# Kernel optimization log

Measured on AMD Instinct MI355X. Metric: run time of the kernel, lower is better.

## Reference

```python
import jax, jax.numpy as jnp
import numpy as np

NUM_HEADS = 16
ROPE_THETA = 10000.0


def apply_rope(x):
    # x: (B, H, T, hd), interleaved-pair RoPE (rotary-embedding-torch convention)
    T, hd = x.shape[-2], x.shape[-1]
    inv_freq = 1.0 / (ROPE_THETA ** (jnp.arange(0, hd, 2, dtype=jnp.float32) / hd))  # (hd/2,)
    ang = jnp.arange(T, dtype=jnp.float32)[:, None] * inv_freq[None, :]  # (T, hd/2)
    cos, sin = jnp.cos(ang), jnp.sin(ang)
    x1 = x[..., 0::2]
    x2 = x[..., 1::2]
    r1 = x1 * cos - x2 * sin
    r2 = x1 * sin + x2 * cos
    return jnp.stack([r1, r2], axis=-1).reshape(x.shape)


def setup_inputs() -> dict:
    key = jax.random.key(0)
    ks = jax.random.split(key, 8)
    L, S, B, E = 2048, 2048, 2, 1024
    sc = 1.0 / np.sqrt(E)
    return {
        "query": jax.random.normal(ks[0], (L, B, E), jnp.float32),
        "key": jax.random.normal(ks[1], (S, B, E), jnp.float32),
        "value": jax.random.normal(ks[2], (S, B, E), jnp.float32),
        "key_padding_mask": jnp.zeros((B, S), dtype=bool),
        "Wq": jax.random.normal(ks[3], (E, E), jnp.float32) * sc,
        "bq": jnp.zeros((E,), jnp.float32),
        "Wk": jax.random.normal(ks[4], (E, E), jnp.float32) * sc,
        "bk": jnp.zeros((E,), jnp.float32),
        "Wv": jax.random.normal(ks[5], (E, E), jnp.float32) * sc,
        "bv": jnp.zeros((E,), jnp.float32),
        "Wo": jax.random.normal(ks[6], (E, E), jnp.float32) * sc,
        "bo": jnp.zeros((E,), jnp.float32),
    }


def reference(query, key, value, key_padding_mask, Wq, bq, Wk, bk, Wv, bv, Wo, bo):
    L, B, E = query.shape
    S = key.shape[0]
    H = NUM_HEADS
    hd = E // H
    # projections (torch Linear: x @ W.T + b)
    Q = query @ Wq.T + bq  # (L, B, E)
    K = key @ Wk.T + bk    # (S, B, E)
    V = value @ Wv.T + bv  # (S, B, E)
    # (T, B, E) -> (B, H, T, hd)
    Q = Q.reshape(L, B, H, hd).transpose(1, 2, 0, 3)
    K = K.reshape(S, B, H, hd).transpose(1, 2, 0, 3)
    V = V.reshape(S, B, H, hd).transpose(1, 2, 0, 3)
    Q = apply_rope(Q)
    K = apply_rope(K)
    scores = jnp.einsum("bhld,bhsd->bhls", Q, K) / jnp.sqrt(jnp.float32(hd))
    scores = jnp.where(key_padding_mask[:, None, None, :], -jnp.inf, scores)
    attn = jax.nn.softmax(scores, axis=-1)
    out = jnp.einsum("bhls,bhsd->bhld", attn, V)  # (B, H, L, hd)
    out = out.transpose(2, 0, 1, 3).reshape(L, B, E)
    return out @ Wo.T + bo
```

## Files before the change

kernel.cpp:

```cpp
#include <hip/hip_runtime.h>
#include <hip/hip_bf16.h>

typedef __hip_bfloat16 bf16;
typedef short bf16x8 __attribute__((ext_vector_type(8)));
typedef float f32x4 __attribute__((ext_vector_type(4)));
typedef short s4 __attribute__((ext_vector_type(4)));

#define LL 2048
#define SS 2048
#define EE 1024
#define HH 16
#define HD 64
#define MM (LL * 2)

static __device__ __forceinline__ short f2bs(float f) {
  bf16 h = __float2bfloat16(f);
  short u;
  __builtin_memcpy(&u, &h, 2);
  return u;
}

#define GLL16(gp, lp) __builtin_amdgcn_global_load_lds(                        \
    (const __attribute__((address_space(1))) void*)(gp),                       \
    (__attribute__((address_space(3))) void*)(lp), 16, 0, 0)

__global__ __launch_bounds__(256) void rope_table_kernel(float2* __restrict__ tab) {
  int i = blockIdx.x * 256 + threadIdx.x;
  int pos = i >> 5, fi = i & 31;
  float freq = expf(-(float)fi * (9.210340371976184f / 32.0f));
  float ang = (float)pos * freq;
  float s, c;
  sincosf(ang, &s, &c);
  tab[i] = make_float2(c, s);
}

__global__ void maskf_kernel(const unsigned char* __restrict__ m,
                             float* __restrict__ mf) {
  int i = blockIdx.x * 256 + threadIdx.x;
  if (i < 2 * SS) mf[i] = m[i] ? -1e30f : 0.f;
}

__global__ __launch_bounds__(256) void cvt_kernel(const float* __restrict__ src,
                                                  bf16* __restrict__ dst) {
  size_t i = ((size_t)blockIdx.x * 256 + threadIdx.x) * 4;
  float4 v = *(const float4*)(src + i);
  s4 p;
  p[0] = f2bs(v.x); p[1] = f2bs(v.y); p[2] = f2bs(v.z); p[3] = f2bs(v.w);
  *(s4*)(dst + i) = p;
}

template<int MODE, bool XB16, bool WB16>
__global__ __launch_bounds__(256) void proj_kernel(
    const void* __restrict__ Xv, const void* __restrict__ Wv,
    const float* __restrict__ bias, void* __restrict__ dstv,
    const float2* __restrict__ tab)
{
  const int w = threadIdx.x >> 6;
  const int lane = threadIdx.x & 63;
  const int l15 = lane & 15, quad = lane >> 4;
  const int tm = blockIdx.x * 128 + w * 32;
  const int tn = blockIdx.y * 64;

  const size_t aoff0 = (size_t)(tm + l15) * EE + quad * 8;
  const size_t aoff1 = aoff0 + (size_t)16 * EE;
  const size_t woff  = (size_t)(tn + l15) * EE + quad * 8;

  f32x4 zero4 = {0.f, 0.f, 0.f, 0.f};
  f32x4 acc[2][4];
#pragma unroll
  for (int mi = 0; mi < 2; ++mi)
#pragma unroll
    for (int ni = 0; ni < 4; ++ni) acc[mi][ni] = zero4;

  for (int k0 = 0; k0 < EE; k0 += 32) {
    bf16x8 a0, a1;
    if (XB16 || MODE == 3) {
      const bf16* Xb = (const bf16*)Xv;
      a0 = *(const bf16x8*)(Xb + aoff0 + k0);
      a1 = *(const bf16x8*)(Xb + aoff1 + k0);
    } else {
      const float* Xf = (const float*)Xv;
#pragma unroll
      for (int j = 0; j < 8; ++j) a0[j] = f2bs(Xf[aoff0 + k0 + j]);
#pragma unroll
      for (int j = 0; j < 8; ++j) a1[j] = f2bs(Xf[aoff1 + k0 + j]);
    }
#pragma unroll
    for (int ni = 0; ni < 4; ++ni) {
      bf16x8 bv;
      if (WB16) {
        const bf16* Wb = (const bf16*)Wv;
        bv = *(const bf16x8*)(Wb + woff + (size_t)ni * 16 * EE + k0);
      } else {
        const float* Wf = (const float*)Wv;
#pragma unroll
        for (int j = 0; j < 8; ++j) bv[j] = f2bs(Wf[woff + (size_t)ni * 16 * EE + k0 + j]);
      }
      acc[0][ni] = __builtin_amdgcn_mfma_f32_16x16x32_bf16(a0, bv, acc[0][ni], 0, 0, 0);
      acc[1][ni] = __builtin_amdgcn_mfma_f32_16x16x32_bf16(a1, bv, acc[1][ni], 0, 0, 0);
    }
  }

  float bz[4];
#pragma unroll
  for (int ni = 0; ni < 4; ++ni) bz[ni] = bias[tn + ni * 16 + l15];

#pragma unroll
  for (int mi = 0; mi < 2; ++mi) {
#pragma unroll
    for (int ni = 0; ni < 4; ++ni) {
      const int n = tn + ni * 16 + l15;
#pragma unroll
      for (int r = 0; r < 4; ++r) {
        const int m = tm + mi * 16 + quad * 4 + r;
        float v = acc[mi][ni][r] + bz[ni];
        if (MODE <= 1) {
          float other = __shfl_xor(v, 1, 64);
          int pos = m >> 1, b = m & 1, d = n & 63, h = n >> 6;
          float2 cs = tab[pos * 32 + (d >> 1)];
          float rv = (d & 1) ? (other * cs.y + v * cs.x) : (v * cs.x - other * cs.y);
          ((bf16*)dstv)[((size_t)(b * HH + h) * LL + pos) * HD + d] = __float2bfloat16(rv);
        } else if (MODE == 2) {
          int pos = m >> 1, b = m & 1, d = n & 63, h = n >> 6;
          ((bf16*)dstv)[((size_t)(b * HH + h) * HD + d) * SS + pos] = __float2bfloat16(v);
        } else {
          ((float*)dstv)[(size_t)m * EE + n] = v;
        }
      }
    }
  }
}

template<int MODE>
__global__ __launch_bounds__(256) void projs_kernel(
    const bf16* __restrict__ X, const bf16* __restrict__ W,
    const float* __restrict__ bias, void* __restrict__ dstv,
    const float2* __restrict__ tab)
{
  __shared__ __align__(16) bf16 As[128 * 32];
  __shared__ __align__(16) bf16 Bs[64 * 32];

  const int tid = threadIdx.x;
  const int w = tid >> 6;
  const int lane = tid & 63;
  const int l15 = lane & 15, quad = lane >> 4;
  const int tmb = blockIdx.x * 128;
  const int tm  = tmb + w * 32;
  const int tn  = blockIdx.y * 64;

  const int srow = tid >> 2;
  const int schk = tid & 3;
  const int gc8  = (schk ^ ((srow >> 1) & 3)) * 8;
  const int swz  = (quad ^ ((l15 >> 1) & 3)) * 8;

  const bf16* gA0 = X + (size_t)(tmb + srow) * EE + gc8;
  const bf16* gA1 = X + (size_t)(tmb + 64 + srow) * EE + gc8;
  const bf16* gB  = W + (size_t)(tn + srow) * EE + gc8;
  bf16* lA0 = As + srow * 32 + schk * 8;
  bf16* lA1 = As + (64 + srow) * 32 + schk * 8;
  bf16* lB  = Bs + srow * 32 + schk * 8;

  f32x4 zero4 = {0.f, 0.f, 0.f, 0.f};
  f32x4 acc[2][4];
#pragma unroll
  for (int mi = 0; mi < 2; ++mi)
#pragma unroll
    for (int ni = 0; ni < 4; ++ni) acc[mi][ni] = zero4;

  for (int k0 = 0; k0 < EE; k0 += 32) {
    GLL16(gA0 + k0, lA0);
    GLL16(gA1 + k0, lA1);
    GLL16(gB + k0, lB);
    __syncthreads();
    bf16x8 af0 = *(const bf16x8*)(As + (w * 32 + l15) * 32 + swz);
    bf16x8 af1 = *(const bf16x8*)(As + (w * 32 + 16 + l15) * 32 + swz);
#pragma unroll
    for (int ni = 0; ni < 4; ++ni) {
      bf16x8 bfr = *(const bf16x8*)(Bs + (ni * 16 + l15) * 32 + swz);
      acc[0][ni] = __builtin_amdgcn_mfma_f32_16x16x32_bf16(af0, bfr, acc[0][ni], 0, 0, 0);
      acc[1][ni] = __builtin_amdgcn_mfma_f32_16x16x32_bf16(af1, bfr, acc[1][ni], 0, 0, 0);
    }
    __syncthreads();
  }

  float bz[4];
#pragma unroll
  for (int ni = 0; ni < 4; ++ni) bz[ni] = bias[tn + ni * 16 + l15];

#pragma unroll
  for (int mi = 0; mi < 2; ++mi) {
#pragma unroll
    for (int ni = 0; ni < 4; ++ni) {
      const int n = tn + ni * 16 + l15;
#pragma unroll
      for (int r = 0; r < 4; ++r) {
        const int m = tm + mi * 16 + quad * 4 + r;
        float v = acc[mi][ni][r] + bz[ni];
        if (MODE <= 1) {
          float other = __shfl_xor(v, 1, 64);
          int pos = m >> 1, b = m & 1, d = n & 63, h = n >> 6;
          float2 cs = tab[pos * 32 + (d >> 1)];
          float rv = (d & 1) ? (other * cs.y + v * cs.x) : (v * cs.x - other * cs.y);
          ((bf16*)dstv)[((size_t)(b * HH + h) * LL + pos) * HD + d] = __float2bfloat16(rv);
        } else if (MODE == 2) {
          int pos = m >> 1, b = m & 1, d = n & 63, h = n >> 6;
          ((bf16*)dstv)[((size_t)(b * HH + h) * HD + d) * SS + pos] = __float2bfloat16(v);
        } else {
          ((float*)dstv)[(size_t)m * EE + n] = v;
        }
      }
    }
  }
}

__global__ __launch_bounds__(256) void attn_kernel(
    const bf16* __restrict__ Qr, const bf16* __restrict__ Kr,
    const bf16* __restrict__ Vt, const float* __restrict__ maskf,
    bf16* __restrict__ ctx)
{
  __shared__ __align__(16) bf16 Ks[2][64 * 64];
  __shared__ __align__(16) bf16 Vs[2][64 * 64];
  __shared__ __align__(16) short Plds[4][32][56];

  const int w = threadIdx.x >> 6;
  const int lane = threadIdx.x & 63;
  const int l15 = lane & 15, quad = lane >> 4;
  const int id = blockIdx.x;
  const int bh = id & 31;
  const int qt = id >> 5;
  const int b = bh >> 4, h = bh & 15;
  const int q0 = qt * 128 + w * 32;

  const bf16* Qbh = Qr + (size_t)bh * LL * HD;
  const bf16* Kbh = Kr + (size_t)bh * SS * HD;
  const bf16* Vbh = Vt + (size_t)bh * HD * SS;
  const float* mrow = maskf + b * SS;

  bf16x8 qf[2][2];
#pragma unroll
  for (int mi = 0; mi < 2; ++mi) {
    const bf16* qp = Qbh + (size_t)(q0 + mi * 16 + l15) * HD + quad * 8;
    qf[mi][0] = *(const bf16x8*)(qp);
    qf[mi][1] = *(const bf16x8*)(qp + 32);
  }

  const int srow = lane >> 3;
  const int gswz = ((lane & 7) ^ srow) * 8;
  const int kswz0 = ((quad    ) ^ (l15 & 7)) * 8;
  const int kswz1 = ((quad + 4) ^ (l15 & 7)) * 8;

#define STAGE(buf, S0) {                                                       \
    _Pragma("unroll")                                                          \
    for (int i = 0; i < 2; ++i) {                                              \
      const int rb = w * 16 + i * 8;                                           \
      GLL16(Kbh + (size_t)((S0) + rb + srow) * HD + gswz,                      \
            (bf16*)&Ks[buf][rb * 64] + lane * 8);                              \
      GLL16(Vbh + (size_t)(rb + srow) * SS + (S0) + gswz,                      \
            (bf16*)&Vs[buf][rb * 64] + lane * 8);                              \
    }                                                                          \
  }

  f32x4 zero4 = {0.f, 0.f, 0.f, 0.f};
  f32x4 o[2][4];
#pragma unroll
  for (int mi = 0; mi < 2; ++mi)
#pragma unroll
    for (int t = 0; t < 4; ++t) o[mi][t] = zero4;
  float ps0 = 0.f, ps1 = 0.f;

  STAGE(0, 0);
  __syncthreads();

  for (int t = 0; t < SS / 64; ++t) {
    const int s0 = t * 64;
    const int cur = t & 1;
    if (t + 1 < SS / 64) STAGE(cur ^ 1, s0 + 64);

#pragma unroll
    for (int ss = 0; ss < 2; ++ss) {
      const bf16* Kb = &Ks[cur][ss * 32 * 64];
      bf16x8 kf00 = *(const bf16x8*)(Kb + (l15)      * 64 + kswz0);
      bf16x8 kf01 = *(const bf16x8*)(Kb + (l15)      * 64 + kswz1);
      bf16x8 kf10 = *(const bf16x8*)(Kb + (16 + l15) * 64 + kswz0);
      bf16x8 kf11 = *(const bf16x8*)(Kb + (16 + l15) * 64 + kswz1);
      bf16x8 vf[4];
#pragma unroll
      for (int tt = 0; tt < 4; ++tt)
        vf[tt] = *(const bf16x8*)(&Vs[cur][0] + (tt * 16 + l15) * 64 +
                                  (((ss * 4 + quad) ^ (l15 & 7)) * 8));
      f32x4 mv0 = *(const f32x4*)(mrow + s0 + ss * 32 + quad * 4);
      f32x4 mv1 = *(const f32x4*)(mrow + s0 + ss * 32 + 16 + quad * 4);

#pragma unroll
      for (int mi = 0; mi < 2; ++mi) {
        f32x4 sc0 = zero4, sc1 = zero4;
        sc0 = __builtin_amdgcn_mfma_f32_16x16x32_bf16(kf00, qf[mi][0], sc0, 0, 0, 0);
        sc0 = __builtin_amdgcn_mfma_f32_16x16x32_bf16(kf01, qf[mi][1], sc0, 0, 0, 0);
        sc1 = __builtin_amdgcn_mfma_f32_16x16x32_bf16(kf10, qf[mi][0], sc1, 0, 0, 0);
        sc1 = __builtin_amdgcn_mfma_f32_16x16x32_bf16(kf11, qf[mi][1], sc1, 0, 0, 0);
        s4 pk0, pk1;
#pragma unroll
        for (int r = 0; r < 4; ++r) {
          float p = __expf(sc0[r] * 0.125f + mv0[r]);
          if (mi == 0) ps0 += p; else ps1 += p;
          pk0[r] = f2bs(p);
        }
#pragma unroll
        for (int r = 0; r < 4; ++r) {
          float p = __expf(sc1[r] * 0.125f + mv1[r]);
          if (mi == 0) ps0 += p; else ps1 += p;
          pk1[r] = f2bs(p);
        }
        *(s4*)&Plds[w][mi * 16 + l15][quad * 4] = pk0;
        *(s4*)&Plds[w][mi * 16 + l15][16 + quad * 4] = pk1;
      }
      asm volatile("" ::: "memory");
      bf16x8 pf0 = *(const bf16x8*)&Plds[w][l15][quad * 8];
      bf16x8 pf1 = *(const bf16x8*)&Plds[w][16 + l15][quad * 8];
#pragma unroll
      for (int tt = 0; tt < 4; ++tt) {
        o[0][tt] = __builtin_amdgcn_mfma_f32_16x16x32_bf16(pf0, vf[tt], o[0][tt], 0, 0, 0);
        o[1][tt] = __builtin_amdgcn_mfma_f32_16x16x32_bf16(pf1, vf[tt], o[1][tt], 0, 0, 0);
      }
      asm volatile("" ::: "memory");
    }
    __syncthreads();
  }
#undef STAGE

  float lv0 = ps0; lv0 += __shfl_xor(lv0, 16, 64); lv0 += __shfl_xor(lv0, 32, 64);
  float lv1 = ps1; lv1 += __shfl_xor(lv1, 16, 64); lv1 += __shfl_xor(lv1, 32, 64);

#pragma unroll
  for (int mi = 0; mi < 2; ++mi) {
#pragma unroll
    for (int r = 0; r < 4; ++r) {
      float lv = (mi == 0) ? lv0 : lv1;
      float li = __shfl(lv, quad * 4 + r, 64);
      float inv = 1.0f / li;
      int q = q0 + mi * 16 + quad * 4 + r;
#pragma unroll
      for (int t = 0; t < 4; ++t) {
        float val = o[mi][t][r] * inv;
        ctx[(size_t)(q * 2 + b) * EE + (size_t)h * 64 + t * 16 + l15] = __float2bfloat16(val);
      }
    }
  }
}

extern "C" void kernel_launch(void* const* d_in, const int* in_sizes, int n_in,
                              void* d_out, int out_size, void* d_ws, size_t ws_size,
                              hipStream_t stream) {
  const float* query = (const float*)d_in[0];
  const float* key   = (const float*)d_in[1];
  const float* value = (const float*)d_in[2];
  const unsigned char* mask = (const unsigned char*)d_in[3];
  const float* Wq = (const float*)d_in[4];
  const float* bq = (const float*)d_in[5];
  const float* Wk = (const float*)d_in[6];
  const float* bk = (const float*)d_in[7];
  const float* Wv = (const float*)d_in[8];
  const float* bv = (const float*)d_in[9];
  const float* Wo = (const float*)d_in[10];
  const float* bo = (const float*)d_in[11];

  char* ws = (char*)d_ws;
  const bool big = ws_size >= ((size_t)41 << 20);

  float2* tab   = (float2*)ws;
  float*  maskf = (float*)(ws + (512 << 10));
  bf16* Wb = (bf16*)(ws + ((size_t)1 << 20));
  bf16* Xb = (bf16*)(ws + ((size_t)9 << 20));
  size_t base = big ? ((size_t)17 << 20) : ((size_t)1 << 20);
  bf16* Qr  = (bf16*)(ws + base);
  bf16* Kr  = (bf16*)(ws + base + ((size_t)8 << 20));
  bf16* Vt  = (bf16*)(ws + base + ((size_t)16 << 20));
  bf16* ctx = big ? Xb : (bf16*)(ws + ((size_t)25 << 20));

  rope_table_kernel<<<(LL * 32) / 256, 256, 0, stream>>>(tab);
  maskf_kernel<<<16, 256, 0, stream>>>(mask, maskf);

  dim3 gp(MM / 128, EE / 64);
  if (big) {
    cvt_kernel<<<1024, 256, 0, stream>>>(Wq, Wb);
    cvt_kernel<<<1024, 256, 0, stream>>>(Wk, Wb + (size_t)EE * EE);
    cvt_kernel<<<1024, 256, 0, stream>>>(Wv, Wb + (size_t)2 * EE * EE);
    cvt_kernel<<<1024, 256, 0, stream>>>(Wo, Wb + (size_t)3 * EE * EE);
    cvt_kernel<<<4096, 256, 0, stream>>>(query, Xb);
    projs_kernel<0><<<gp, 256, 0, stream>>>(Xb, Wb, bq, Qr, tab);
    cvt_kernel<<<4096, 256, 0, stream>>>(key, Xb);
    projs_kernel<1><<<gp, 256, 0, stream>>>(Xb, Wb + (size_t)EE * EE, bk, Kr, tab);
    cvt_kernel<<<4096, 256, 0, stream>>>(value, Xb);
    projs_kernel<2><<<gp, 256, 0, stream>>>(Xb, Wb + (size_t)2 * EE * EE, bv, Vt, tab);
  } else {
    proj_kernel<0, false, false><<<gp, 256, 0, stream>>>(query, Wq, bq, Qr, tab);
    proj_kernel<1, false, false><<<gp, 256, 0, stream>>>(key,   Wk, bk, Kr, tab);
    proj_kernel<2, false, false><<<gp, 256, 0, stream>>>(value, Wv, bv, Vt, tab);
  }

  attn_kernel<<<(LL / 128) * 2 * HH, 256, 0, stream>>>(Qr, Kr, Vt, maskf, ctx);

  if (big) projs_kernel<3><<<gp, 256, 0, stream>>>(ctx, Wb + (size_t)3 * EE * EE, bo, d_out, tab);
  else     proj_kernel<3, true, false><<<gp, 256, 0, stream>>>(ctx, Wo, bo, d_out, tab);
}
```

Baseline: 270.7 us.

## Double-buffer projection GEMM with 64-wide K tiles and fuse setup kernels

The shared-memory projection GEMM now uses two LDS buffers with a K tile of 64 instead of 32, prefetching the next tile via global_load_lds while the current one feeds MFMAs. This halves the number of K-loop iterations, cuts the barriers per iteration from two to one, and hides global load latency. It uses a new XOR swizzle across 8 chunks and more LDS. Separately, the rope-table and mask kernels are merged into one launch, and the four weight conversions are merged into a single cvt4 launch to reduce launch overhead.

Result: no change. 265.9 us (-1.8%).

```diff
diff --git a/kernel.cpp b/kernel.cpp
--- a/kernel.cpp
+++ b/kernel.cpp
@@ -24,20 +24,21 @@
     (const __attribute__((address_space(1))) void*)(gp),                       \
     (__attribute__((address_space(3))) void*)(lp), 16, 0, 0)
 
-__global__ __launch_bounds__(256) void rope_table_kernel(float2* __restrict__ tab) {
-  int i = blockIdx.x * 256 + threadIdx.x;
-  int pos = i >> 5, fi = i & 31;
-  float freq = expf(-(float)fi * (9.210340371976184f / 32.0f));
-  float ang = (float)pos * freq;
-  float s, c;
-  sincosf(ang, &s, &c);
-  tab[i] = make_float2(c, s);
-}
-
-__global__ void maskf_kernel(const unsigned char* __restrict__ m,
-                             float* __restrict__ mf) {
-  int i = blockIdx.x * 256 + threadIdx.x;
-  if (i < 2 * SS) mf[i] = m[i] ? -1e30f : 0.f;
+__global__ __launch_bounds__(256) void tables_kernel(
+    float2* __restrict__ tab, const unsigned char* __restrict__ m,
+    float* __restrict__ mf) {
+  if (blockIdx.x < 256) {
+    int i = blockIdx.x * 256 + threadIdx.x;
+    int pos = i >> 5, fi = i & 31;
+    float freq = expf(-(float)fi * (9.210340371976184f / 32.0f));
+    float ang = (float)pos * freq;
+    float s, c;
+    sincosf(ang, &s, &c);
+    tab[i] = make_float2(c, s);
+  } else {
+    int i = (blockIdx.x - 256) * 256 + threadIdx.x;
+    if (i < 2 * SS) mf[i] = m[i] ? -1e30f : 0.f;
+  }
 }
 
 __global__ __launch_bounds__(256) void cvt_kernel(const float* __restrict__ src,
@@ -47,6 +48,19 @@
   s4 p;
   p[0] = f2bs(v.x); p[1] = f2bs(v.y); p[2] = f2bs(v.z); p[3] = f2bs(v.w);
   *(s4*)(dst + i) = p;
+}
+
+__global__ __launch_bounds__(256) void cvt4_kernel(
+    const float* __restrict__ s0, const float* __restrict__ s1,
+    const float* __restrict__ s2, const float* __restrict__ s3,
+    bf16* __restrict__ dst) {
+  int sel = blockIdx.x >> 10;
+  const float* src = (sel == 0) ? s0 : (sel == 1) ? s1 : (sel == 2) ? s2 : s3;
+  size_t loc = ((size_t)(blockIdx.x & 1023) * 256 + threadIdx.x) * 4;
+  float4 v = *(const float4*)(src + loc);
+  s4 p;
+  p[0] = f2bs(v.x); p[1] = f2bs(v.y); p[2] = f2bs(v.z); p[3] = f2bs(v.w);
+  *(s4*)(dst + (size_t)sel * EE * EE + loc) = p;
 }
 
 template<int MODE, bool XB16, bool WB16>
@@ -137,8 +151,8 @@
     const float* __restrict__ bias, void* __restrict__ dstv,
     const float2* __restrict__ tab)
 {
-  __shared__ __align__(16) bf16 As[128 * 32];
-  __shared__ __align__(16) bf16 Bs[64 * 32];
+  __shared__ __align__(16) bf16 As[2][128 * 64];
+  __shared__ __align__(16) bf16 Bs[2][64 * 64];
 
   const int tid = threadIdx.x;
   const int w = tid >> 6;
@@ -148,17 +162,23 @@
   const int tm  = tmb + w * 32;
   const int tn  = blockIdx.y * 64;
 
-  const int srow = tid >> 2;
-  const int schk = tid & 3;
-  const int gc8  = (schk ^ ((srow >> 1) & 3)) * 8;
-  const int swz  = (quad ^ ((l15 >> 1) & 3)) * 8;
-
-  const bf16* gA0 = X + (size_t)(tmb + srow) * EE + gc8;
-  const bf16* gA1 = X + (size_t)(tmb + 64 + srow) * EE + gc8;
-  const bf16* gB  = W + (size_t)(tn + srow) * EE + gc8;
-  bf16* lA0 = As + srow * 32 + schk * 8;
-  bf16* lA1 = As + (64 + srow) * 32 + schk * 8;
-  bf16* lB  = Bs + srow * 32 + schk * 8;
+  const int srow = lane >> 3;
+  const int sgc  = ((lane & 7) ^ srow) * 8;
+
+#define PSTAGE(buf, K0) {                                                      \
+    _Pragma("unroll")                                                          \
+    for (int i = 0; i < 4; ++i) {                                              \
+      const int rb = w * 32 + i * 8;                                           \
+      GLL16(X + (size_t)(tmb + rb + srow) * EE + (K0) + sgc,                   \
+            (bf16*)&As[buf][rb * 64] + lane * 8);                              \
+    }                                                                          \
+    _Pragma("unroll")                                                          \
+    for (int i = 0; i < 2; ++i) {                                              \
+      const int rb = w * 16 + i * 8;                                           \
+      GLL16(W + (size_t)(tn + rb + srow) * EE + (K0) + sgc,                    \
+            (bf16*)&Bs[buf][rb * 64] + lane * 8);                              \
+    }                                                                          \
+  }
 
   f32x4 zero4 = {0.f, 0.f, 0.f, 0.f};
   f32x4 acc[2][4];
@@ -167,21 +187,27 @@
 #pragma unroll
     for (int ni = 0; ni < 4; ++ni) acc[mi][ni] = zero4;
 
-  for (int k0 = 0; k0 < EE; k0 += 32) {
-    GLL16(gA0 + k0, lA0);
-    GLL16(gA1 + k0, lA1);
-    GLL16(gB + k0, lB);
+  PSTAGE(0, 0);
+  __syncthreads();
+
+  for (int t = 0; t < EE / 64; ++t) {
+    const int cur = t & 1;
+    if (t + 1 < EE / 64) PSTAGE(cur ^ 1, (t + 1) * 64);
+#pragma unroll
+    for (int ks = 0; ks < 2; ++ks) {
+      const int rsw = ((ks * 4 + quad) ^ (l15 & 7)) * 8;
+      bf16x8 a0 = *(const bf16x8*)(&As[cur][0] + (w * 32 + l15) * 64 + rsw);
+      bf16x8 a1 = *(const bf16x8*)(&As[cur][0] + (w * 32 + 16 + l15) * 64 + rsw);
+#pragma unroll
+      for (int ni = 0; ni < 4; ++ni) {
+        bf16x8 bfr = *(const bf16x8*)(&Bs[cur][0] + (ni * 16 + l15) * 64 + rsw);
+        acc[0][ni] = __builtin_amdgcn_mfma_f32_16x16x32_bf16(a0, bfr, acc[0][ni], 0, 0, 0);
+        acc[1][ni] = __builtin_amdgcn_mfma_f32_16x16x32_bf16(a1, bfr, acc[1][ni], 0, 0, 0);
+      }
+    }
     __syncthreads();
-    bf16x8 af0 = *(const bf16x8*)(As + (w * 32 + l15) * 32 + swz);
-    bf16x8 af1 = *(const bf16x8*)(As + (w * 32 + 16 + l15) * 32 + swz);
-#pragma unroll
-    for (int ni = 0; ni < 4; ++ni) {
-      bf16x8 bfr = *(const bf16x8*)(Bs + (ni * 16 + l15) * 32 + swz);
-      acc[0][ni] = __builtin_amdgcn_mfma_f32_16x16x32_bf16(af0, bfr, acc[0][ni], 0, 0, 0);
-      acc[1][ni] = __builtin_amdgcn_mfma_f32_16x16x32_bf16(af1, bfr, acc[1][ni], 0, 0, 0);
-    }
-    __syncthreads();
-  }
+  }
+#undef PSTAGE
 
   float bz[4];
 #pragma unroll
@@ -377,15 +403,11 @@
   bf16* Vt  = (bf16*)(ws + base + ((size_t)16 << 20));
   bf16* ctx = big ? Xb : (bf16*)(ws + ((size_t)25 << 20));
 
-  rope_table_kernel<<<(LL * 32) / 256, 256, 0, stream>>>(tab);
-  maskf_kernel<<<16, 256, 0, stream>>>(mask, maskf);
+  tables_kernel<<<272, 256, 0, stream>>>(tab, mask, maskf);
 
   dim3 gp(MM / 128, EE / 64);
   if (big) {
-    cvt_kernel<<<1024, 256, 0, stream>>>(Wq, Wb);
-    cvt_kernel<<<1024, 256, 0, stream>>>(Wk, Wb + (size_t)EE * EE);
-    cvt_kernel<<<1024, 256, 0, stream>>>(Wv, Wb + (size_t)2 * EE * EE);
-    cvt_kernel<<<1024, 256, 0, stream>>>(Wo, Wb + (size_t)3 * EE * EE);
+    cvt4_kernel<<<4096, 256, 0, stream>>>(Wq, Wk, Wv, Wo, Wb);
     cvt_kernel<<<4096, 256, 0, stream>>>(query, Xb);
     projs_kernel<0><<<gp, 256, 0, stream>>>(Xb, Wb, bq, Qr, tab);
     cvt_kernel<<<4096, 256, 0, stream>>>(key, Xb);
```
